# Optimization experiments

Measured on AMD Instinct MI355X. Metric: run time of the kernel, lower is better.

The kernel has to match this reference:

```python
import jax, jax.numpy as jnp
import numpy as np

G = 8            # group_order
KS = 3           # kernel size
C1, O1 = 1, 16   # gconv1 channels
C2, O2 = 16, 32  # gconv2 channels
HW = 28
NUM_CLASSES = 10


def _bilinear_sample(img, px, py):
    # img: (O, I, K, K); px, py: (K, K) pixel coords; zero padding outside
    # (matches torch grid_sample bilinear, align_corners=False, padding_mode='zeros')
    K = img.shape[-1]
    x0 = jnp.floor(px); y0 = jnp.floor(py)
    wx = px - x0; wy = py - y0
    x0i = x0.astype(jnp.int32); y0i = y0.astype(jnp.int32)

    def gather(yi, xi):
        valid = (yi >= 0) & (yi < K) & (xi >= 0) & (xi < K)
        yc = jnp.clip(yi, 0, K - 1)
        xc = jnp.clip(xi, 0, K - 1)
        return img[:, :, yc, xc] * valid.astype(img.dtype)  # (O,I,K,K)

    return (gather(y0i, x0i) * (1 - wx) * (1 - wy)
            + gather(y0i, x0i + 1) * wx * (1 - wy)
            + gather(y0i + 1, x0i) * (1 - wx) * wy
            + gather(y0i + 1, x0i + 1) * wx * wy)


def _rotated_kernels(base, group_order):
    # Replicates F.affine_grid + F.grid_sample (align_corners=False) for each rotation k.
    K = base.shape[-1]
    coords = (2.0 * jnp.arange(K, dtype=base.dtype) + 1.0) / K - 1.0  # normalized centers
    xs, ys = jnp.meshgrid(coords, coords, indexing='xy')  # x along width, y along height

    def rot_k(k):
        theta = 2.0 * np.pi * k / group_order
        c, s = jnp.cos(theta), jnp.sin(theta)
        gx = c * xs - s * ys   # theta row [cos, -sin, 0]
        gy = s * xs + c * ys   # theta row [sin,  cos, 0]
        px = ((gx + 1.0) * K - 1.0) / 2.0  # unnormalize, align_corners=False
        py = ((gy + 1.0) * K - 1.0) / 2.0
        return _bilinear_sample(base, px, py)

    return jax.vmap(rot_k)(jnp.arange(group_order, dtype=base.dtype))  # (G,O,I,K,K)


def _conv2d(x, w, pad):
    return jax.lax.conv_general_dilated(
        x, w, window_strides=(1, 1), padding=[(pad, pad), (pad, pad)],
        dimension_numbers=('NCHW', 'OIHW', 'NCHW'))


def setup_inputs() -> dict:
    key = jax.random.key(0)
    k1, k2, k3, k4, k5 = jax.random.split(key, 5)
    x = jax.random.normal(k1, (512, C1, HW, HW), dtype=jnp.float32)
    base_weight = jax.random.normal(k2, (O1, C1, KS, KS), dtype=jnp.float32)
    w2 = jax.random.normal(k3, (O2, C2, G, KS, KS), dtype=jnp.float32) * 0.05
    fc_w = jax.random.normal(k4, (NUM_CLASSES, O2 * HW * HW), dtype=jnp.float32) * 0.01
    fc_b = jax.random.normal(k5, (NUM_CLASSES,), dtype=jnp.float32) * 0.01
    return {"x": x, "base_weight": base_weight, "w2": w2, "fc_w": fc_w, "fc_b": fc_b}


def reference(x, base_weight, w2, fc_w, fc_b):
    B = x.shape[0]
    # --- GroupConv2D: steerable rotated kernels, concat along out-channels (k-major) ---
    rk = _rotated_kernels(base_weight, G)           # (G, O1, C1, K, K)
    w1 = rk.reshape(G * O1, C1, KS, KS)
    h = _conv2d(x, w1, 1)                           # (B, G*O1, 28, 28)
    h = jax.nn.relu(h)                              # GroupReLU == plain ReLU

    # --- GroupToGroupConv: circulant structure fused into one conv ---
    # torch: out channel = g*O2 + o (cat dim=1), in channel = c*G + h_idx (view layout)
    g = jnp.arange(G)[:, None]
    hh = jnp.arange(G)[None, :]
    idx = (g - hh) % G                               # (G, G)
    Wc = w2[:, :, idx]                               # (O2, C2, G_g, G_h, K, K)
    Wbig = jnp.transpose(Wc, (2, 0, 1, 3, 4, 5)).reshape(G * O2, C2 * G, KS, KS)
    h2 = _conv2d(h, Wbig, 1)                         # (B, G*O2, 28, 28)
    h2 = jax.nn.relu(h2)

    # --- GroupPooling (mean over the *inner* factor of 8, as in the torch view) ---
    p = h2.reshape(B, (G * O2) // G, G, HW, HW).mean(axis=2)  # (B, 32, 28, 28)

    # --- fc ---
    flat = p.reshape(B, -1)
    return flat @ fc_w.T + fc_b
```

## Files before the change

kernel.cpp:

```cpp
#include <hip/hip_runtime.h>
#include <hip/hip_bf16.h>
#include <cstdint>

#define AS1 __attribute__((address_space(1)))
#define AS3 __attribute__((address_space(3)))

typedef __bf16 bf16x8 __attribute__((ext_vector_type(8)));
typedef float  f32x16 __attribute__((ext_vector_type(16)));

__device__ __forceinline__ void gld_lds16(const void* g, void* l) {
    __builtin_amdgcn_global_load_lds((const AS1 void*)g, (AS3 void*)l, 16, 0, 0);
}

__global__ __launch_bounds__(256) void k_conv1(const float* __restrict__ x,
                                               const float* __restrict__ base,
                                               const float* __restrict__ w2,
                                               __hip_bfloat16* __restrict__ hl,
                                               __hip_bfloat16* __restrict__ A) {
    int tid = threadIdx.x;

    if (blockIdx.x < 1152) {
        int i = blockIdx.x * 256 + tid;
        int r = i / 1152, k = i - r * 1152;
        int g = r >> 5, o2 = r & 31;
        int kk = k >> 7, cch = k & 127;
        int ky = kk / 3, kx = kk - ky * 3;
        int c2 = cch >> 3, hh = cch & 7;
        int gi = (g - hh) & 7;
        A[i] = __float2bfloat16(w2[((o2 * 16 + c2) * 8 + gi) * 9 + ky * 3 + kx]);
    }

    __shared__ float w1s[1152];
    if (tid < 128) {
        int g = tid >> 4, o = tid & 15;
        float th = 6.28318530717958647692f * (float)g / 8.0f;
        float c = cosf(th), s = sinf(th);
        for (int i = 0; i < 3; ++i) {
            float ys = (2.0f * i + 1.0f) / 3.0f - 1.0f;
            for (int j = 0; j < 3; ++j) {
                float xs = (2.0f * j + 1.0f) / 3.0f - 1.0f;
                float gx = c * xs - s * ys;
                float gy = s * xs + c * ys;
                float px = ((gx + 1.0f) * 3.0f - 1.0f) * 0.5f;
                float py = ((gy + 1.0f) * 3.0f - 1.0f) * 0.5f;
                float x0 = floorf(px), y0 = floorf(py);
                float wx = px - x0, wy = py - y0;
                int x0i = (int)x0, y0i = (int)y0;
                auto gat = [&](int yi, int xi) -> float {
                    bool v = (yi >= 0) && (yi < 3) && (xi >= 0) && (xi < 3);
                    int yc = min(max(yi, 0), 2), xc = min(max(xi, 0), 2);
                    return v ? base[o * 9 + yc * 3 + xc] : 0.0f;
                };
                w1s[tid * 9 + i * 3 + j] =
                      gat(y0i, x0i)         * (1.0f - wx) * (1.0f - wy)
                    + gat(y0i, x0i + 1)     * wx          * (1.0f - wy)
                    + gat(y0i + 1, x0i)     * (1.0f - wx) * wy
                    + gat(y0i + 1, x0i + 1) * wx          * wy;
            }
        }
    }
    __syncthreads();

    const int c0 = (tid & 15) * 8;
    float wreg[8][9];
#pragma unroll
    for (int cc = 0; cc < 8; ++cc)
#pragma unroll
        for (int k = 0; k < 9; ++k) wreg[cc][k] = w1s[(c0 + cc) * 9 + k];

    const int ps = tid >> 4;
    const int pbase = blockIdx.x * 64;

#pragma unroll
    for (int j = 0; j < 4; ++j) {
        int pi = pbase + j * 16 + ps;
        int xx = pi % 30; int t = pi / 30; int yy = t % 30; int b = t / 30;
        float acc[8] = {0.f,0.f,0.f,0.f,0.f,0.f,0.f,0.f};
        if (xx >= 1 && xx <= 28 && yy >= 1 && yy <= 28) {
            const float* xb = x + b * 784;
            int y = yy - 1, xc = xx - 1;
#pragma unroll
            for (int dy = -1; dy <= 1; ++dy) {
                int sy = y + dy;
#pragma unroll
                for (int dx = -1; dx <= 1; ++dx) {
                    int sx = xc + dx;
                    float xv = (sy >= 0 && sy < 28 && sx >= 0 && sx < 28) ? xb[sy * 28 + sx] : 0.0f;
                    int k = (dy + 1) * 3 + (dx + 1);
#pragma unroll
                    for (int cc = 0; cc < 8; ++cc) acc[cc] += xv * wreg[cc][k];
                }
            }
        }
        union { __hip_bfloat16 h[8]; float4 f4; } u;
#pragma unroll
        for (int cc = 0; cc < 8; ++cc) u.h[cc] = __float2bfloat16(fmaxf(acc[cc], 0.0f));
        *(float4*)(hl + (size_t)pi * 128 + c0) = u.f4;
    }
}

__global__ __launch_bounds__(256) void k_conv2(const __hip_bfloat16* __restrict__ A,
                                               const __hip_bfloat16* __restrict__ hl,
                                               float* __restrict__ p) {
    __shared__ __align__(16) char smem[32768];

    const int tid  = threadIdx.x;
    const int lane = tid & 63;
    const int w    = tid >> 6;
    const int wr   = w >> 1, wc = w & 1;
    const int hi   = lane >> 5;

    const int bid  = blockIdx.x;
    const int xcd  = bid & 7;
    const int slot = bid >> 3;
    const int nt   = xcd + 8 * (slot >> 1);
    const int mt   = slot & 1;
    const int n0 = nt << 7;
    const int r0 = mt << 7;

    uint32_t aG[4], bG[4], ldsOff[4];
#pragma unroll
    for (int q = 0; q < 4; ++q) {
        int ch = w * 4 + q;
        int rl = ch * 8 + (lane >> 3);
        int ca = (lane & 7) ^ (rl & 7);
        aG[q] = (uint32_t)((r0 + rl) * 2304 + ca * 16);
        int n  = n0 + rl;
        int b  = n / 784; int rr = n - b * 784;
        int y  = rr / 28; int xx = rr - y * 28;
        bG[q]  = (uint32_t)(((b * 30 + y) * 30 + xx) * 256 + ca * 16);
        ldsOff[q] = (uint32_t)(ch * 1024);
    }

    uint32_t aro[2], bro[2]; int asw[2], bsw[2];
#pragma unroll
    for (int t = 0; t < 2; ++t) {
        int rl = 64 * wr + 32 * t + (lane & 31);
        aro[t] = (uint32_t)(rl * 128); asw[t] = rl & 7;
        int nl = 64 * wc + 32 * t + (lane & 31);
        bro[t] = (uint32_t)(16384 + nl * 128); bsw[t] = nl & 7;
    }

    f32x16 acc[2][2];
#pragma unroll
    for (int i = 0; i < 2; ++i)
#pragma unroll
        for (int j = 0; j < 2; ++j) acc[i][j] = (f32x16)(0.0f);

    const char* Ab = (const char*)A;
    const char* Hb = (const char*)hl;

    for (int s = 0; s < 18; ++s) {
        int kk = s >> 1, half = s & 1;
        int ky = kk / 3, kx = kk - ky * 3;
        int aoff = kk * 256 + half * 128;
        int boff = (ky * 30 + kx) * 256 + half * 128;

        __syncthreads();
#pragma unroll
        for (int q = 0; q < 4; ++q) {
            gld_lds16(Ab + aG[q] + aoff, smem + ldsOff[q]);
            gld_lds16(Hb + bG[q] + boff, smem + 16384 + ldsOff[q]);
        }
        __syncthreads();

#pragma unroll
        for (int kstep = 0; kstep < 4; ++kstep) {
            int cb = kstep * 2 + hi;
            bf16x8 af[2], bf[2];
#pragma unroll
            for (int t = 0; t < 2; ++t) {
                af[t] = *(const bf16x8*)(smem + aro[t] + ((cb ^ asw[t]) * 16));
                bf[t] = *(const bf16x8*)(smem + bro[t] + ((cb ^ bsw[t]) * 16));
            }
#pragma unroll
            for (int i = 0; i < 2; ++i)
#pragma unroll
                for (int j = 0; j < 2; ++j)
                    acc[i][j] = __builtin_amdgcn_mfma_f32_32x32x16_bf16(af[i], bf[j], acc[i][j], 0, 0, 0);
        }
    }

#pragma unroll
    for (int ti = 0; ti < 2; ++ti) {
        int gbase = (r0 + 64 * wr + 32 * ti) >> 3;
#pragma unroll
        for (int tj = 0; tj < 2; ++tj) {
            f32x16 v = acc[ti][tj];
#pragma unroll
            for (int q = 0; q < 4; ++q) {
                float s = fmaxf(v[4*q], 0.0f) + fmaxf(v[4*q+1], 0.0f)
                        + fmaxf(v[4*q+2], 0.0f) + fmaxf(v[4*q+3], 0.0f);
                s += __shfl_xor(s, 32, 64);
                if (hi == 0) {
                    int a = gbase + q;
                    int n = n0 + 64 * wc + 32 * tj + (lane & 31);
                    int b = n / 784; int rr = n - b * 784;
                    p[(b * 32 + a) * 784 + rr] = s * 0.125f;
                }
            }
        }
    }
}

__global__ __launch_bounds__(256) void k_fc(const float* __restrict__ p,
                                            const float* __restrict__ fw,
                                            const float* __restrict__ fb,
                                            float* __restrict__ out) {
    int b = blockIdx.x >> 2, ks = blockIdx.x & 3;
    int tid = threadIdx.x;
    const float4* p4 = (const float4*)(p + (size_t)b * 25088);
    const float4* w4 = (const float4*)fw;
    float acc[10] = {};
    for (int i = ks * 1568 + tid; i < (ks + 1) * 1568; i += 256) {
        float4 v = p4[i];
#pragma unroll
        for (int c = 0; c < 10; ++c) {
            float4 u = w4[c * 6272 + i];
            acc[c] += v.x * u.x + v.y * u.y + v.z * u.z + v.w * u.w;
        }
    }
    __shared__ float red[10][4];
    int lane = tid & 63, wv = tid >> 6;
#pragma unroll
    for (int c = 0; c < 10; ++c) {
        float s = acc[c];
#pragma unroll
        for (int o = 32; o > 0; o >>= 1) s += __shfl_down(s, o, 64);
        if (lane == 0) red[c][wv] = s;
    }
    __syncthreads();
    if (tid < 10) {
        float s = red[tid][0] + red[tid][1] + red[tid][2] + red[tid][3];
        if (ks == 0) s += fb[tid];
        atomicAdd(&out[b * 10 + tid], s);
    }
}

extern "C" void kernel_launch(void* const* d_in, const int* in_sizes, int n_in,
                              void* d_out, int out_size, void* d_ws, size_t ws_size,
                              hipStream_t stream) {
    const float* x  = (const float*)d_in[0];
    const float* bw = (const float*)d_in[1];
    const float* w2 = (const float*)d_in[2];
    const float* fw = (const float*)d_in[3];
    const float* fb = (const float*)d_in[4];
    float* out = (float*)d_out;
    char* ws = (char*)d_ws;

    __hip_bfloat16* Amat = (__hip_bfloat16*)(ws + 4608);
    __hip_bfloat16* hl   = (__hip_bfloat16*)(ws + 594432);
    float*          p    = (float*)(ws + 118563328);

    hipMemsetAsync(d_out, 0, (size_t)out_size * sizeof(float), stream);
    k_conv1<<<7200, 256, 0, stream>>>(x, bw, w2, hl, Amat);
    k_conv2<<<6272, 256, 0, stream>>>(Amat, hl, p);
    k_fc   <<<2048, 256, 0, stream>>>(p, fw, fb, out);
}
```

Measured before the change: 396.5 us.

## Register-tile conv1, store pooled activations as bf16, adjust LDS swizzle

Conv1 now maps each thread to four adjacent output pixels in a row band and loads a 3x6 input window into registers once, reusing it across the 3x3 taps instead of reloading per pixel. The grid grows so each batch image is covered by 15 two-row bands. The pooled output p is written and read as bf16 instead of fp32, which halves that intermediate's write and read traffic in conv2 and fc, at some cost in precision. The conv2 LDS swizzle adds an extra XOR term, aimed at reducing bank conflicts.

After: 376.1 us. -5.1%, faster.

```diff
diff --git a/kernel.cpp b/kernel.cpp
--- a/kernel.cpp
+++ b/kernel.cpp
@@ -68,40 +68,63 @@
 #pragma unroll
         for (int k = 0; k < 9; ++k) wreg[cc][k] = w1s[(c0 + cc) * 9 + k];
 
-    const int ps = tid >> 4;
-    const int pbase = blockIdx.x * 64;
+    const int slot = tid >> 4;
+    const int band = blockIdx.x % 15;
+    const int b    = blockIdx.x / 15;
+    const int yy   = band * 2 + (slot >> 3);
+    const int xx0  = (slot & 7) * 4;
+
+    const float* xb = x + b * 784;
+    float xv[3][6];
+#pragma unroll
+    for (int t = 0; t < 3; ++t) {
+        int sy = yy - 2 + t;
+        bool syok = (sy >= 0) && (sy < 28);
+#pragma unroll
+        for (int u = 0; u < 6; ++u) {
+            int sx = xx0 - 2 + u;
+            bool ok = syok && (sx >= 0) && (sx < 28);
+            xv[t][u] = ok ? xb[sy * 28 + sx] : 0.0f;
+        }
+    }
+
+    float acc[4][8];
+#pragma unroll
+    for (int j = 0; j < 4; ++j)
+#pragma unroll
+        for (int cc = 0; cc < 8; ++cc) acc[j][cc] = 0.0f;
+
+#pragma unroll
+    for (int t = 0; t < 3; ++t)
+#pragma unroll
+        for (int u = 0; u < 3; ++u) {
+#pragma unroll
+            for (int j = 0; j < 4; ++j) {
+                float xvv = xv[t][j + u];
+#pragma unroll
+                for (int cc = 0; cc < 8; ++cc)
+                    acc[j][cc] += xvv * wreg[cc][t * 3 + u];
+            }
+        }
 
 #pragma unroll
     for (int j = 0; j < 4; ++j) {
-        int pi = pbase + j * 16 + ps;
-        int xx = pi % 30; int t = pi / 30; int yy = t % 30; int b = t / 30;
-        float acc[8] = {0.f,0.f,0.f,0.f,0.f,0.f,0.f,0.f};
-        if (xx >= 1 && xx <= 28 && yy >= 1 && yy <= 28) {
-            const float* xb = x + b * 784;
-            int y = yy - 1, xc = xx - 1;
-#pragma unroll
-            for (int dy = -1; dy <= 1; ++dy) {
-                int sy = y + dy;
-#pragma unroll
-                for (int dx = -1; dx <= 1; ++dx) {
-                    int sx = xc + dx;
-                    float xv = (sy >= 0 && sy < 28 && sx >= 0 && sx < 28) ? xb[sy * 28 + sx] : 0.0f;
-                    int k = (dy + 1) * 3 + (dx + 1);
-#pragma unroll
-                    for (int cc = 0; cc < 8; ++cc) acc[cc] += xv * wreg[cc][k];
-                }
-            }
-        }
-        union { __hip_bfloat16 h[8]; float4 f4; } u;
-#pragma unroll
-        for (int cc = 0; cc < 8; ++cc) u.h[cc] = __float2bfloat16(fmaxf(acc[cc], 0.0f));
-        *(float4*)(hl + (size_t)pi * 128 + c0) = u.f4;
+        int xx = xx0 + j;
+        if (xx < 30) {
+            bool interior = (yy >= 1) && (yy <= 28) && (xx >= 1) && (xx <= 28);
+            union { __hip_bfloat16 h[8]; float4 f4; } u;
+#pragma unroll
+            for (int cc = 0; cc < 8; ++cc)
+                u.h[cc] = __float2bfloat16(interior ? fmaxf(acc[j][cc], 0.0f) : 0.0f);
+            int pi = b * 900 + yy * 30 + xx;
+            *(float4*)(hl + (size_t)pi * 128 + c0) = u.f4;
+        }
     }
 }
 
 __global__ __launch_bounds__(256) void k_conv2(const __hip_bfloat16* __restrict__ A,
                                                const __hip_bfloat16* __restrict__ hl,
-                                               float* __restrict__ p) {
+                                               __hip_bfloat16* __restrict__ p) {
     __shared__ __align__(16) char smem[32768];
 
     const int tid  = threadIdx.x;
@@ -123,7 +146,7 @@
     for (int q = 0; q < 4; ++q) {
         int ch = w * 4 + q;
         int rl = ch * 8 + (lane >> 3);
-        int ca = (lane & 7) ^ (rl & 7);
+        int ca = (lane & 7) ^ (rl & 7) ^ (ch & 3);
         aG[q] = (uint32_t)((r0 + rl) * 2304 + ca * 16);
         int n  = n0 + rl;
         int b  = n / 784; int rr = n - b * 784;
@@ -136,9 +159,9 @@
 #pragma unroll
     for (int t = 0; t < 2; ++t) {
         int rl = 64 * wr + 32 * t + (lane & 31);
-        aro[t] = (uint32_t)(rl * 128); asw[t] = rl & 7;
+        aro[t] = (uint32_t)(rl * 128); asw[t] = (rl & 7) ^ ((rl >> 3) & 3);
         int nl = 64 * wc + 32 * t + (lane & 31);
-        bro[t] = (uint32_t)(16384 + nl * 128); bsw[t] = nl & 7;
+        bro[t] = (uint32_t)(16384 + nl * 128); bsw[t] = (nl & 7) ^ ((nl >> 3) & 3);
     }
 
     f32x16 acc[2][2];
@@ -196,28 +219,34 @@
                     int a = gbase + q;
                     int n = n0 + 64 * wc + 32 * tj + (lane & 31);
                     int b = n / 784; int rr = n - b * 784;
-                    p[(b * 32 + a) * 784 + rr] = s * 0.125f;
+                    p[(b * 32 + a) * 784 + rr] = __float2bfloat16(s * 0.125f);
                 }
             }
         }
     }
 }
 
-__global__ __launch_bounds__(256) void k_fc(const float* __restrict__ p,
+__global__ __launch_bounds__(256) void k_fc(const __hip_bfloat16* __restrict__ p,
                                             const float* __restrict__ fw,
                                             const float* __restrict__ fb,
                                             float* __restrict__ out) {
     int b = blockIdx.x >> 2, ks = blockIdx.x & 3;
     int tid = threadIdx.x;
-    const float4* p4 = (const float4*)(p + (size_t)b * 25088);
+    const bf16x8* pb = (const bf16x8*)(p + (size_t)b * 25088);
     const float4* w4 = (const float4*)fw;
     float acc[10] = {};
-    for (int i = ks * 1568 + tid; i < (ks + 1) * 1568; i += 256) {
-        float4 v = p4[i];
+    for (int t = ks * 784 + tid; t < (ks + 1) * 784; t += 256) {
+        union { bf16x8 v; __hip_bfloat16 h[8]; } u;
+        u.v = pb[t];
+        float vf[8];
+#pragma unroll
+        for (int e = 0; e < 8; ++e) vf[e] = __bfloat162float(u.h[e]);
 #pragma unroll
         for (int c = 0; c < 10; ++c) {
-            float4 u = w4[c * 6272 + i];
-            acc[c] += v.x * u.x + v.y * u.y + v.z * u.z + v.w * u.w;
+            float4 u0 = w4[c * 6272 + 2 * t];
+            float4 u1 = w4[c * 6272 + 2 * t + 1];
+            acc[c] += vf[0] * u0.x + vf[1] * u0.y + vf[2] * u0.z + vf[3] * u0.w
+                    + vf[4] * u1.x + vf[5] * u1.y + vf[6] * u1.z + vf[7] * u1.w;
         }
     }
     __shared__ float red[10][4];
@@ -250,10 +279,10 @@
 
     __hip_bfloat16* Amat = (__hip_bfloat16*)(ws + 4608);
     __hip_bfloat16* hl   = (__hip_bfloat16*)(ws + 594432);
-    float*          p    = (float*)(ws + 118563328);
+    __hip_bfloat16* p    = (__hip_bfloat16*)(ws + 118563328);
 
     hipMemsetAsync(d_out, 0, (size_t)out_size * sizeof(float), stream);
-    k_conv1<<<7200, 256, 0, stream>>>(x, bw, w2, hl, Amat);
+    k_conv1<<<7680, 256, 0, stream>>>(x, bw, w2, hl, Amat);
     k_conv2<<<6272, 256, 0, stream>>>(Amat, hl, p);
     k_fc   <<<2048, 256, 0, stream>>>(p, fw, fb, out);
 }
```
